# Optimization experiments

Hardware: AMD Instinct MI355X
Metric: run time of the kernel (lower is better)

The kernel has to match this reference:

```python
import jax, jax.numpy as jnp
import numpy as np

NEIGHBORS_FOR_LRF = 128
NEIGHBORS_FOR_AVG = 128
EPS = 1e-12  # safe-sqrt epsilon (self-distance is exactly 0)


def _pairwise_dist(v):
    # v: [N, 3] -> [N, N] euclidean distances
    sq = jnp.sum(v * v, axis=-1)
    d2 = sq[:, None] - 2.0 * (v @ v.T) + sq[None, :]
    return jnp.sqrt(jnp.maximum(d2, EPS))


def _shot_lrf(neighborhoods, radius):
    # neighborhoods: [N, K, 3] (centered at query point); radius: [N]
    d = jnp.sqrt(jnp.maximum(jnp.sum(neighborhoods * neighborhoods, axis=-1), EPS))  # [N, K]
    w = radius[:, None] - d  # SHOT weights (radius - distance)
    cov = jnp.einsum("nk,nki,nkj->nij", w, neighborhoods, neighborhoods)
    cov = cov / jnp.sum(w, axis=-1)[:, None, None]  # [N, 3, 3]
    _, vecs = jnp.linalg.eigh(cov)  # ascending eigenvalues; eigenvectors in columns
    x = vecs[:, :, 2]  # largest-eigenvalue direction
    z = vecs[:, :, 0]  # smallest-eigenvalue direction (normal)
    # SHOT sign disambiguation: orient toward the majority of neighbors
    xp = jnp.einsum("nki,ni->nk", neighborhoods, x)
    x = jnp.where((jnp.sum(xp >= 0, axis=-1) >= jnp.sum(xp < 0, axis=-1))[:, None], x, -x)
    zp = jnp.einsum("nki,ni->nk", neighborhoods, z)
    z = jnp.where((jnp.sum(zp >= 0, axis=-1) >= jnp.sum(zp < 0, axis=-1))[:, None], z, -z)
    y = jnp.cross(z, x)
    return jnp.stack([z, y, x], axis=1)  # [N, 3, 3]; row 0 = normal


def _per_sample(v):
    # v: [N, 3]
    D = _pairwise_dist(v)  # [N, N]
    neg_d, idx = jax.lax.top_k(-D, NEIGHBORS_FOR_LRF)  # nearest K (incl. self)
    radii = -neg_d  # [N, K], ascending distances
    radius = radii[:, -1]  # per-neighborhood support radius
    neighborhoods = v[idx] - v[:, None, :]  # [N, K, 3]
    lrfs = _shot_lrf(neighborhoods, radius)
    normals = lrfs[:, 0, :]  # [N, 3]
    avg = jnp.mean(normals[idx[:, :NEIGHBORS_FOR_AVG]], axis=1)  # gather + mean
    return avg / jnp.linalg.norm(avg, axis=-1, keepdims=True)


def setup_inputs() -> dict:
    key = jax.random.key(0)
    vertices = jax.random.normal(key, (2, 8192, 3), dtype=jnp.float32)
    return {"vertices": vertices}


def reference(vertices) -> jnp.ndarray:
    # tf.map_fn over batch -> vmap
    return jax.vmap(_per_sample)(vertices)  # [B, N, 3] averaged unit normals
```

## Files before the change

kernel.cpp:

```cpp
#include <hip/hip_runtime.h>

#define NPTS 8192
#define KNN  128
#define TPB  256
#define WPB  4
#define CANDCAP 384


__device__ __forceinline__ float f_signf(float a, float b){ return copysignf(a, b); }

__device__ float lapy2f(float x, float y){
#pragma clang fp contract(off)
  float xa = fabsf(x), ya = fabsf(y);
  float w = fmaxf(xa, ya), zz = fminf(xa, ya);
  if (zz == 0.0f) return w;
  float t = zz / w;
  return w * sqrtf(1.0f + t * t);
}

__device__ void slartg_(float f, float g, float &c, float &s, float &r){
#pragma clang fp contract(off)
  const float safmin = 1.17549435e-38f;
  const float safmax = 8.5070592e37f;
  if (g == 0.0f){ c = 1.0f; s = 0.0f; r = f; }
  else if (f == 0.0f){ c = 0.0f; s = f_signf(1.0f, g); r = fabsf(g); }
  else {
    float f1 = fabsf(f), g1 = fabsf(g);
    float rtmin = sqrtf(safmin);
    float rtmax = sqrtf(safmax * 0.5f);
    if (f1 > rtmin && f1 < rtmax && g1 > rtmin && g1 < rtmax){
      float d = sqrtf(f * f + g * g);
      float p = 1.0f / d;
      c = f1 * p;
      s = g * f_signf(p, f);
      r = f_signf(d, f);
    } else {
      float u = fminf(safmax, fmaxf(safmin, fmaxf(f1, g1)));
      float uu = 1.0f / u;
      float fs = f * uu, gs = g * uu;
      float d = sqrtf(fs * fs + gs * gs);
      float p = 1.0f / d;
      c = fabsf(fs) * p;
      s = gs * f_signf(p, f);
      r = f_signf(d, f) * u;
    }
  }
}

__device__ void slaev2_(float a, float b, float cc, float &rt1, float &rt2,
                        float &cs1, float &sn1){
#pragma clang fp contract(off)
  float sm = a + cc;
  float df = a - cc;
  float adf = fabsf(df);
  float tb = b + b;
  float ab = fabsf(tb);
  float acmx, acmn;
  if (fabsf(a) > fabsf(cc)){ acmx = a; acmn = cc; } else { acmx = cc; acmn = a; }
  float rt;
  if (adf > ab){ float t = ab / adf; rt = adf * sqrtf(1.0f + t * t); }
  else if (adf < ab){ float t = adf / ab; rt = ab * sqrtf(1.0f + t * t); }
  else { rt = ab * sqrtf(2.0f); }
  int sgn1;
  if (sm < 0.0f){ rt1 = 0.5f * (sm - rt); sgn1 = -1; rt2 = (acmx / rt1) * acmn - (b / rt1) * b; }
  else if (sm > 0.0f){ rt1 = 0.5f * (sm + rt); sgn1 = 1; rt2 = (acmx / rt1) * acmn - (b / rt1) * b; }
  else { rt1 = 0.5f * rt; rt2 = -0.5f * rt; sgn1 = 1; }
  float cs; int sgn2;
  if (df >= 0.0f){ cs = df + rt; sgn2 = 1; }
  else { cs = df - rt; sgn2 = -1; }
  float acs = fabsf(cs);
  if (acs > ab){
    float ct = -tb / cs;
    sn1 = 1.0f / sqrtf(1.0f + ct * ct);
    cs1 = ct * sn1;
  } else {
    if (ab == 0.0f){ cs1 = 1.0f; sn1 = 0.0f; }
    else {
      float tn = -cs / tb;
      cs1 = 1.0f / sqrtf(1.0f + tn * tn);
      sn1 = tn * cs1;
    }
  }
  if (sgn1 == sgn2){ float tn = cs1; cs1 = -sn1; sn1 = tn; }
}

__device__ void ssteqr3(float *d, float *e, float z[3][3]){
#pragma clang fp contract(off)
  const float eps  = 5.9604645e-8f;
  const float eps2 = 3.5527137e-15f;
  const float safmin = 1.17549435e-38f;
  const int n = 3;
  for (int i = 0; i < 3; i++)
    for (int j = 0; j < 3; j++) z[i][j] = (i == j) ? 1.0f : 0.0f;
  const int nmaxit = n * 30;
  int jtot = 0;
  int l1 = 1;
  int l = 0, lsv = 0, lend = 0, lendsv = 0, m = 0;
  float p, g, r, c, s, f, b;
  float csave[2], ssave[2];
  int safety = 0;

L10:
  if (++safety > 64) goto L190;
  if (l1 > n) goto L160;
  if (l1 > 1) e[l1 - 2] = 0.0f;
  if (l1 <= n - 1){
    for (m = l1; m <= n - 1; m++){
      float tst = fabsf(e[m - 1]);
      if (tst == 0.0f) goto L30;
      if (tst <= (sqrtf(fabsf(d[m - 1])) * sqrtf(fabsf(d[m]))) * eps){ e[m - 1] = 0.0f; goto L30; }
    }
  }
  m = n;
L30:
  l = l1; lsv = l; lend = m; lendsv = lend; l1 = m + 1;
  if (lend == l) goto L10;
  {
    float anorm = fabsf(d[l - 1]);
    for (int q = l; q <= lend - 1; q++){
      anorm = fmaxf(anorm, fabsf(d[q]));
      anorm = fmaxf(anorm, fabsf(e[q - 1]));
    }
    if (anorm == 0.0f) goto L10;
  }
  if (fabsf(d[lend - 1]) < fabsf(d[l - 1])){ lend = lsv; l = lendsv; }
  if (lend > l){
L40:
    if (l != lend){
      for (m = l; m <= lend - 1; m++){
        float tst = e[m - 1] * e[m - 1];
        if (tst <= (eps2 * fabsf(d[m - 1])) * fabsf(d[m]) + safmin) goto L60;
      }
    }
    m = lend;
L60:
    if (m < lend) e[m - 1] = 0.0f;
    p = d[l - 1];
    if (m == l) goto L80;
    if (m == l + 1){
      float rt1, rt2;
      slaev2_(d[l - 1], e[l - 1], d[l], rt1, rt2, c, s);
      for (int i2 = 0; i2 < 3; i2++){
        float temp = z[i2][l];
        z[i2][l]     = c * temp - s * z[i2][l - 1];
        z[i2][l - 1] = s * temp + c * z[i2][l - 1];
      }
      d[l - 1] = rt1; d[l] = rt2; e[l - 1] = 0.0f;
      l += 2;
      if (l <= lend) goto L40;
      goto L140;
    }
    if (jtot == nmaxit) goto L140;
    jtot++;
    g = (d[l] - p) / (2.0f * e[l - 1]);
    r = lapy2f(g, 1.0f);
    g = d[m - 1] - p + e[l - 1] / (g + f_signf(r, g));
    s = 1.0f; c = 1.0f; p = 0.0f;
    for (int i2 = m - 1; i2 >= l; i2--){
      f = s * e[i2 - 1];
      b = c * e[i2 - 1];
      slartg_(g, f, c, s, r);
      if (i2 != m - 1) e[i2] = r;
      g = d[i2] - p;
      r = (d[i2 - 1] - g) * s + 2.0f * c * b;
      p = s * r;
      d[i2] = g + p;
      g = c * r - b;
      csave[i2 - l] = c; ssave[i2 - l] = -s;
    }
    {
      int mmc = m - l + 1;
      for (int j2 = mmc - 1; j2 >= 1; j2--){
        float cj = csave[j2 - 1], sj = ssave[j2 - 1];
        if (cj != 1.0f || sj != 0.0f){
          for (int i2 = 0; i2 < 3; i2++){
            float temp = z[i2][(l - 1) + j2];
            z[i2][(l - 1) + j2]     = cj * temp - sj * z[i2][(l - 1) + j2 - 1];
            z[i2][(l - 1) + j2 - 1] = sj * temp + cj * z[i2][(l - 1) + j2 - 1];
          }
        }
      }
    }
    d[l - 1] -= p;
    e[l - 1] = g;
    goto L40;
L80:
    d[l - 1] = p;
    l++;
    if (l <= lend) goto L40;
    goto L140;
  } else {
L90:
    if (l != lend){
      for (m = l; m >= lend + 1; m--){
        float tst = e[m - 2] * e[m - 2];
        if (tst <= (eps2 * fabsf(d[m - 1])) * fabsf(d[m - 2]) + safmin) goto L110;
      }
    }
    m = lend;
L110:
    if (m > lend) e[m - 2] = 0.0f;
    p = d[l - 1];
    if (m == l) goto L130;
    if (m == l - 1){
      float rt1, rt2;
      slaev2_(d[l - 2], e[l - 2], d[l - 1], rt1, rt2, c, s);
      for (int i2 = 0; i2 < 3; i2++){
        float temp = z[i2][l - 1];
        z[i2][l - 1] = c * temp - s * z[i2][l - 2];
        z[i2][l - 2] = s * temp + c * z[i2][l - 2];
      }
      d[l - 2] = rt1; d[l - 1] = rt2; e[l - 2] = 0.0f;
      l -= 2;
      if (l >= lend) goto L90;
      goto L140;
    }
    if (jtot == nmaxit) goto L140;
    jtot++;
    g = (d[l - 2] - p) / (2.0f * e[l - 2]);
    r = lapy2f(g, 1.0f);
    g = d[m - 1] - p + e[l - 2] / (g + f_signf(r, g));
    s = 1.0f; c = 1.0f; p = 0.0f;
    for (int i2 = m; i2 <= l - 1; i2++){
      f = s * e[i2 - 1];
      b = c * e[i2 - 1];
      slartg_(g, f, c, s, r);
      if (i2 != m) e[i2 - 2] = r;
      g = d[i2 - 1] - p;
      r = (d[i2] - g) * s + 2.0f * c * b;
      p = s * r;
      d[i2 - 1] = g + p;
      g = c * r - b;
      csave[i2 - m] = c; ssave[i2 - m] = s;
    }
    {
      int cnt = l - m + 1;
      for (int j2 = 1; j2 <= cnt - 1; j2++){
        float cj = csave[j2 - 1], sj = ssave[j2 - 1];
        if (cj != 1.0f || sj != 0.0f){
          for (int i2 = 0; i2 < 3; i2++){
            float temp = z[i2][(m - 1) + j2];
            z[i2][(m - 1) + j2]     = cj * temp - sj * z[i2][(m - 1) + j2 - 1];
            z[i2][(m - 1) + j2 - 1] = sj * temp + cj * z[i2][(m - 1) + j2 - 1];
          }
        }
      }
    }
    d[l - 1] -= p;
    e[l - 2] = g;
    goto L90;
L130:
    d[l - 1] = p;
    l--;
    if (l >= lend) goto L90;
    goto L140;
  }
L140:
  if (jtot < nmaxit) goto L10;
  goto L190;
L160:
  for (int ii = 2; ii <= n; ii++){
    int i2 = ii - 1, k2 = i2;
    float pp = d[i2 - 1];
    for (int j2 = ii; j2 <= n; j2++){
      if (d[j2 - 1] < pp){ k2 = j2; pp = d[j2 - 1]; }
    }
    if (k2 != i2){
      d[k2 - 1] = d[i2 - 1]; d[i2 - 1] = pp;
      for (int r2 = 0; r2 < 3; r2++){
        float tt = z[r2][i2 - 1]; z[r2][i2 - 1] = z[r2][k2 - 1]; z[r2][k2 - 1] = tt;
      }
    }
  }
L190: ;
}

__device__ void eigh3_smallest_f32(const float A6[6], float zout[3]){
#pragma clang fp contract(off)
  float a00 = A6[0], a10 = A6[1], a20 = A6[2], a11 = A6[3], a21 = A6[4], a22 = A6[5];
  float d[3], e[2], tau1 = 0.0f, v2 = 0.0f;
  float xnorm = fabsf(a20);
  if (xnorm == 0.0f){
    tau1 = 0.0f;
    d[0] = a00; d[1] = a11; d[2] = a22; e[0] = a10; e[1] = a21;
  } else {
    float alpha = a10;
    float beta = -f_signf(lapy2f(alpha, xnorm), alpha);
    tau1 = (beta - alpha) / beta;
    float rsc = 1.0f / (alpha - beta);
    v2 = a20 * rsc;
    float y1 = tau1 * a11 + tau1 * (a21 * v2);
    float y2 = tau1 * a21 + (tau1 * v2) * a22;
    float dotv = y1 + y2 * v2;
    float al = (-0.5f * tau1) * dotv;
    float w1 = y1 + al;
    float w2 = y2 + al * v2;
    d[0] = a00;
    d[1] = (a11 + (-w1)) + (w1 * (-1.0f));
    e[1] = (a21 + v2 * (-w1)) + (w2 * (-1.0f));
    d[2] = (a22 + v2 * (-w2)) + (w2 * (-v2));
    e[0] = beta;
  }
  float z[3][3];
  ssteqr3(d, e, z);
  if (tau1 != 0.0f){
    for (int j = 0; j < 3; j++){
      float wj = z[1][j] + z[2][j] * v2;
      float tmp = (-tau1) * wj;
      z[1][j] = z[1][j] + tmp;
      z[2][j] = z[2][j] + v2 * tmp;
    }
  }
  zout[0] = z[0][0]; zout[1] = z[1][0]; zout[2] = z[2][0];
}

__device__ __forceinline__ void wsync(){
  asm volatile("s_waitcnt lgkmcnt(0)" ::: "memory");
}
__device__ __forceinline__ unsigned int wscan_incl(unsigned int v, int lane){
  #pragma unroll
  for (int off = 1; off < 64; off <<= 1){
    unsigned int n = (unsigned int)__shfl_up((int)v, off, 64);
    if (lane >= off) v += n;
  }
  return v;
}
__device__ __forceinline__ unsigned int lanepos(unsigned long long bal){
  return __builtin_amdgcn_mbcnt_hi((unsigned int)(bal >> 32),
         __builtin_amdgcn_mbcnt_lo((unsigned int)bal, 0u));
}

#define DBITS(A_, B_, C_, SQJ_, OUT_) { \
  float dot_ = fmaf(vz, (C_), fmaf(vy, (B_), vx * (A_))); \
  float d2_ = (sqi - 2.0f * dot_) + (SQJ_); \
  float D_ = sqrtf(fmaxf(d2_, 1e-12f)); \
  OUT_ = __float_as_uint(D_); }

__global__ __launch_bounds__(256) void sq_kernel(const float* __restrict__ verts,
                                                 float* __restrict__ sqbuf, int total)
{
#pragma clang fp contract(off)
  int g = blockIdx.x * 256 + threadIdx.x;
  if (g < total){
    float a = verts[3 * g + 0], b = verts[3 * g + 1], c = verts[3 * g + 2];
    sqbuf[g] = (a * a + b * b) + c * c;
  }
}

__global__ __launch_bounds__(TPB, 8) void phase1_kernel(const float* __restrict__ verts,
                                                        const float* __restrict__ sqbuf,
                                                        float* __restrict__ normals,
                                                        unsigned short* __restrict__ idx_out)
{
#pragma clang fp contract(off)
  __shared__ unsigned long long regionA[WPB][CANDCAP];
  __shared__ float4 regionB[WPB][KNN];

  const int t    = threadIdx.x;
  const int w    = t >> 6;
  const int lane = t & 63;
  const int gq   = blockIdx.x * WPB + w;
  const int smp  = gq >> 13;
  const int i    = gq & (NPTS - 1);
  const float* V  = verts + (size_t)smp * NPTS * 3;
  const float* SQ = sqbuf + (size_t)smp * NPTS;

  unsigned long long* cand = &regionA[w][0];
  unsigned int* hist = (unsigned int*)cand;
  unsigned long long* skey = (unsigned long long*)&regionB[w][0];
  float4* nbf = &regionB[w][0];

  const float vx = V[3 * i + 0], vy = V[3 * i + 1], vz = V[3 * i + 2];
  const float sqi = SQ[i];

  unsigned int prefix = 0u, kt = KNN, cnt = 0u;
  int shift = 19, pshift = 32, stop_shift = 19;
  for (int level = 0; level < 4; level++){
    #pragma unroll
    for (int z2 = 0; z2 < 8; z2++) hist[z2 * 64 + lane] = 0u;
    wsync();
    const unsigned int dmask = (unsigned int)((1 << (pshift - shift)) - 1);
    #pragma unroll 2
    for (int k = 0; k < NPTS / 256; k++){
      const int j0 = k * 256 + lane * 4;
      const float4* Vp = (const float4*)(V + 3 * j0);
      float4 fa = Vp[0], fb = Vp[1], fc = Vp[2];
      float4 sj = *(const float4*)(SQ + j0);
      float px[4] = {fa.x, fa.w, fb.z, fc.y};
      float py[4] = {fa.y, fb.x, fb.w, fc.z};
      float pz[4] = {fa.z, fb.y, fc.x, fc.w};
      float ps[4] = {sj.x, sj.y, sj.z, sj.w};
      #pragma unroll
      for (int s = 0; s < 4; s++){
        unsigned int bits; DBITS(px[s], py[s], pz[s], ps[s], bits);
        if (level == 0){
          int v = (int)(bits >> 19) - 1696;
          unsigned int dig = (unsigned int)(v < 0 ? 0 : (v > 511 ? 511 : v));
          atomicAdd(&hist[dig], 1u);
        } else if ((bits >> pshift) == prefix){
          atomicAdd(&hist[(bits >> shift) & dmask], 1u);
        }
      }
    }
    wsync();
    unsigned int hh[8], inc[8], tot[8];
    #pragma unroll
    for (int s = 0; s < 8; s++){
      hh[s] = hist[s * 64 + lane];
      inc[s] = wscan_incl(hh[s], lane);
      tot[s] = (unsigned int)__shfl((int)inc[s], 63, 64);
    }
    unsigned int selb = 0xffffffffu, nkt = 0u, ncnt = 0u, basep = 0u;
    #pragma unroll
    for (int s = 0; s < 8; s++){
      unsigned int gincl = inc[s] + basep;
      unsigned int gexcl = gincl - hh[s];
      if (hh[s] > 0u && gexcl < kt && kt <= gincl){
        selb = (unsigned int)(s * 64 + lane); nkt = kt - gexcl; ncnt = hh[s];
      }
      basep += tot[s];
    }
    unsigned long long bal = __ballot(selb != 0xffffffffu);
    int src = (int)(__ffsll((long long)bal) - 1);
    selb = (unsigned int)__shfl((int)selb, src, 64);
    nkt  = (unsigned int)__shfl((int)nkt,  src, 64);
    ncnt = (unsigned int)__shfl((int)ncnt, src, 64);
    prefix = (level == 0) ? (selb + 1696u) : ((prefix << (pshift - shift)) | selb);
    kt = nkt; cnt = ncnt; stop_shift = shift;
    if (cnt <= 256u) break;
    pshift = shift;
    shift = (shift == 19) ? 11 : ((shift == 11) ? 3 : 0);
  }

  unsigned int base = 0u;
  #pragma unroll 2
  for (int k = 0; k < NPTS / 256; k++){
    const int j0 = k * 256 + lane * 4;
    const float4* Vp = (const float4*)(V + 3 * j0);
    float4 fa = Vp[0], fb = Vp[1], fc = Vp[2];
    float4 sj = *(const float4*)(SQ + j0);
    float px[4] = {fa.x, fa.w, fb.z, fc.y};
    float py[4] = {fa.y, fb.x, fb.w, fc.z};
    float pz[4] = {fa.z, fb.y, fc.x, fc.w};
    float ps[4] = {sj.x, sj.y, sj.z, sj.w};
    #pragma unroll
    for (int s = 0; s < 4; s++){
      unsigned int bits; DBITS(px[s], py[s], pz[s], ps[s], bits);
      bool pred = ((bits >> stop_shift) <= prefix);
      unsigned long long bal = __ballot(pred);
      if (pred){
        unsigned int p = base + lanepos(bal);
        if (p < CANDCAP) cand[p] = (((unsigned long long)bits) << 13) | (unsigned long long)(j0 + s);
      }
      base += (unsigned int)__popcll(bal);
    }
  }
  wsync();
  unsigned int candN = base; if (candN > CANDCAP) candN = CANDCAP;

  for (unsigned int c = lane; c < candN; c += 64){
    unsigned long long key = cand[c];
    unsigned int rank = 0u;
    #pragma unroll 4
    for (unsigned int jj = 0; jj < candN; jj++) rank += (cand[jj] < key) ? 1u : 0u;
    if (rank < KNN) skey[rank] = key;
  }
  wsync();

  const float radius = __uint_as_float((unsigned int)(skey[KNN - 1] >> 13));
  unsigned long long k0 = skey[lane];
  unsigned long long k1 = skey[lane + 64];
  wsync();
  {
    int j0 = (int)(k0 & 8191ULL);
    float a = V[3 * j0 + 0] - vx;
    float b = V[3 * j0 + 1] - vy;
    float c = V[3 * j0 + 2] - vz;
    float dd2 = (a * a + b * b) + c * c;
    nbf[lane] = make_float4(a, b, c, radius - sqrtf(fmaxf(dd2, 1e-12f)));
    idx_out[(size_t)gq * KNN + lane] = (unsigned short)j0;
  }
  {
    int j1 = (int)(k1 & 8191ULL);
    float a = V[3 * j1 + 0] - vx;
    float b = V[3 * j1 + 1] - vy;
    float c = V[3 * j1 + 2] - vz;
    float dd2 = (a * a + b * b) + c * c;
    nbf[lane + 64] = make_float4(a, b, c, radius - sqrtf(fmaxf(dd2, 1e-12f)));
    idx_out[(size_t)gq * KNN + 64 + lane] = (unsigned short)j1;
  }
  wsync();

  float acc = 0.0f;
  if (lane < 6){
    #pragma unroll 4
    for (int k = 0; k < KNN; k++){
      float4 nb4 = nbf[k];
      float wn = nb4.w, x = nb4.x, y = nb4.y, zc = nb4.z;
      float u = (lane == 0) ? x : ((lane == 1 || lane == 3) ? y : zc);
      float v = (lane < 3) ? x : ((lane < 5) ? y : zc);
      acc += (wn * u) * v;
    }
  } else if (lane == 6){
    float r8[8];
    for (int q = 0; q < 8; q++) r8[q] = nbf[q].w;
    for (int k = 8; k < KNN; k += 8)
      for (int q = 0; q < 8; q++) r8[q] += nbf[k + q].w;
    acc = ((r8[0] + r8[1]) + (r8[2] + r8[3])) + ((r8[4] + r8[5]) + (r8[6] + r8[7]));
  }
  float c00 = __shfl(acc, 0, 64), c10 = __shfl(acc, 1, 64), c20 = __shfl(acc, 2, 64);
  float c11 = __shfl(acc, 3, 64), c21 = __shfl(acc, 4, 64), c22 = __shfl(acc, 5, 64);
  float wsum = __shfl(acc, 6, 64);

  float A6[6];
  A6[0] = c00 / wsum; A6[1] = c10 / wsum; A6[2] = c20 / wsum;
  A6[3] = c11 / wsum; A6[4] = c21 / wsum; A6[5] = c22 / wsum;
  float zv[3];
  eigh3_smallest_f32(A6, zv);

  float4 q0 = nbf[lane], q1 = nbf[lane + 64];
  float zp0 = ((q0.x * zv[0]) + (q0.y * zv[1])) + (q0.z * zv[2]);
  float zp1 = ((q1.x * zv[0]) + (q1.y * zv[1])) + (q1.z * zv[2]);
  unsigned int votes = (unsigned int)__popcll(__ballot(zp0 >= 0.0f))
                     + (unsigned int)__popcll(__ballot(zp1 >= 0.0f));
  float sg = (votes >= (unsigned)(KNN - votes)) ? 1.0f : -1.0f;
  if (lane == 0){
    normals[(size_t)gq * 3 + 0] = sg * zv[0];
    normals[(size_t)gq * 3 + 1] = sg * zv[1];
    normals[(size_t)gq * 3 + 2] = sg * zv[2];
  }
}

__global__ __launch_bounds__(TPB) void phase2_kernel(const float* __restrict__ normals,
                                                     const unsigned short* __restrict__ idx_in,
                                                     float* __restrict__ out)
{
#pragma clang fp contract(off)
  const int t    = threadIdx.x;
  const int w    = t >> 6;
  const int lane = t & 63;
  const int g    = blockIdx.x * WPB + w;
  const int smp  = g >> 13;
  const int base = smp << 13;
  const int j0 = (int)idx_in[(size_t)g * KNN + lane];
  const int j1 = (int)idx_in[(size_t)g * KNN + 64 + lane];
  const float* n0 = normals + (size_t)(base + j0) * 3;
  const float* n1 = normals + (size_t)(base + j1) * 3;
  float a0 = n0[0] + n1[0];
  float a1 = n0[1] + n1[1];
  float a2 = n0[2] + n1[2];
  #pragma unroll
  for (int off = 32; off > 0; off >>= 1){
    a0 += __shfl_down(a0, off, 64);
    a1 += __shfl_down(a1, off, 64);
    a2 += __shfl_down(a2, off, 64);
  }
  if (lane == 0){
    a0 /= 128.0f; a1 /= 128.0f; a2 /= 128.0f;
    float nrm = sqrtf(((a0 * a0) + (a1 * a1)) + (a2 * a2));
    out[(size_t)g * 3 + 0] = a0 / nrm;
    out[(size_t)g * 3 + 1] = a1 / nrm;
    out[(size_t)g * 3 + 2] = a2 / nrm;
  }
}

extern "C" void kernel_launch(void* const* d_in, const int* in_sizes, int n_in,
                              void* d_out, int out_size, void* d_ws, size_t ws_size,
                              hipStream_t stream){
  const float* verts = (const float*)d_in[0];
  float* out = (float*)d_out;
  const int total = in_sizes[0] / 3;
  float* normals = (float*)d_ws;
  unsigned short* idxb = (unsigned short*)((char*)d_ws + (size_t)total * 3 * sizeof(float));
  float* sqbuf = (float*)((char*)d_ws + (size_t)total * 3 * sizeof(float)
                                       + (size_t)total * KNN * sizeof(unsigned short));
  sq_kernel<<<dim3((total + 255) / 256), dim3(256), 0, stream>>>(verts, sqbuf, total);
  phase1_kernel<<<dim3(total / WPB), dim3(TPB), 0, stream>>>(verts, sqbuf, normals, idxb);
  phase2_kernel<<<dim3(total / WPB), dim3(TPB), 0, stream>>>(normals, idxb, out);
}
```

Before: 269.5 us.

## Stage candidate point tiles in shared memory across block warps

Each block now cooperatively loads 1024-point tiles of vertices and squared norms into shared memory, and all four warps scan them from LDS instead of each warp streaming the full point set from global memory. The radix-select histogram passes and the candidate-collection pass both use the tiles. This needs block-wide barriers per tile and a block-level vote so all warps keep looping until every warp has finished selection. The cost is extra syncs, warps that have finished still joining tile loads, and 16KB more shared memory, which may lower occupancy.

```diff
diff --git a/kernel.cpp b/kernel.cpp
--- a/kernel.cpp
+++ b/kernel.cpp
@@ -4,6 +4,7 @@
 #define KNN  128
 #define TPB  256
 #define WPB  4
+#define TILE 1024
 #define CANDCAP 384
 
 
@@ -353,8 +354,10 @@
                                                         unsigned short* __restrict__ idx_out)
 {
 #pragma clang fp contract(off)
+  __shared__ float4 tileMem[TILE];
   __shared__ unsigned long long regionA[WPB][CANDCAP];
   __shared__ float4 regionB[WPB][KNN];
+  __shared__ unsigned int sh_cont;
 
   const int t    = threadIdx.x;
   const int w    = t >> 6;
@@ -364,6 +367,8 @@
   const int i    = gq & (NPTS - 1);
   const float* V  = verts + (size_t)smp * NPTS * 3;
   const float* SQ = sqbuf + (size_t)smp * NPTS;
+  const float* tV  = (const float*)tileMem;
+  const float* tSQ = (const float*)tileMem + 3 * TILE;
 
   unsigned long long* cand = &regionA[w][0];
   unsigned int* hist = (unsigned int*)cand;
@@ -375,17 +380,108 @@
 
   unsigned int prefix = 0u, kt = KNN, cnt = 0u;
   int shift = 19, pshift = 32, stop_shift = 19;
+  bool done = false;
   for (int level = 0; level < 4; level++){
+    if (!done){
+      #pragma unroll
+      for (int z2 = 0; z2 < 8; z2++) hist[z2 * 64 + lane] = 0u;
+    }
+    const unsigned int dmask = (unsigned int)((1 << (pshift - shift)) - 1);
+    for (int tb = 0; tb < NPTS; tb += TILE){
+      __syncthreads();
+      {
+        const float4* vsrc = (const float4*)(V + 3 * tb);
+        const float4* qsrc = (const float4*)(SQ + tb);
+        tileMem[t]       = vsrc[t];
+        tileMem[256 + t] = vsrc[256 + t];
+        tileMem[512 + t] = vsrc[512 + t];
+        tileMem[768 + t] = qsrc[t];
+      }
+      __syncthreads();
+      if (!done){
+        #pragma unroll
+        for (int k = 0; k < TILE / 256; k++){
+          const int j0 = k * 256 + lane * 4;
+          const float4* Vp = (const float4*)(tV + 3 * j0);
+          float4 fa = Vp[0], fb = Vp[1], fc = Vp[2];
+          float4 sj = *(const float4*)(tSQ + j0);
+          float px[4] = {fa.x, fa.w, fb.z, fc.y};
+          float py[4] = {fa.y, fb.x, fb.w, fc.z};
+          float pz[4] = {fa.z, fb.y, fc.x, fc.w};
+          float ps[4] = {sj.x, sj.y, sj.z, sj.w};
+          #pragma unroll
+          for (int s = 0; s < 4; s++){
+            unsigned int bits; DBITS(px[s], py[s], pz[s], ps[s], bits);
+            if (level == 0){
+              int v = (int)(bits >> 19) - 1696;
+              unsigned int dig = (unsigned int)(v < 0 ? 0 : (v > 511 ? 511 : v));
+              atomicAdd(&hist[dig], 1u);
+            } else if ((bits >> pshift) == prefix){
+              atomicAdd(&hist[(bits >> shift) & dmask], 1u);
+            }
+          }
+        }
+      }
+    }
+    if (!done){
+      wsync();
+      unsigned int hh[8], inc[8], tot[8];
+      #pragma unroll
+      for (int s = 0; s < 8; s++){
+        hh[s] = hist[s * 64 + lane];
+        inc[s] = wscan_incl(hh[s], lane);
+        tot[s] = (unsigned int)__shfl((int)inc[s], 63, 64);
+      }
+      unsigned int selb = 0xffffffffu, nkt = 0u, ncnt = 0u, basep = 0u;
+      #pragma unroll
+      for (int s = 0; s < 8; s++){
+        unsigned int gincl = inc[s] + basep;
+        unsigned int gexcl = gincl - hh[s];
+        if (hh[s] > 0u && gexcl < kt && kt <= gincl){
+          selb = (unsigned int)(s * 64 + lane); nkt = kt - gexcl; ncnt = hh[s];
+        }
+        basep += tot[s];
+      }
+      unsigned long long bal = __ballot(selb != 0xffffffffu);
+      int src = (int)(__ffsll((long long)bal) - 1);
+      selb = (unsigned int)__shfl((int)selb, src, 64);
+      nkt  = (unsigned int)__shfl((int)nkt,  src, 64);
+      ncnt = (unsigned int)__shfl((int)ncnt, src, 64);
+      prefix = (level == 0) ? (selb + 1696u) : ((prefix << (pshift - shift)) | selb);
+      kt = nkt; cnt = ncnt; stop_shift = shift;
+      if (cnt <= 256u || level == 3){
+        done = true;
+      } else {
+        pshift = shift;
+        shift = (shift == 19) ? 11 : ((shift == 11) ? 3 : 0);
+      }
+    }
+    if (t == 0) sh_cont = 0u;
+    __syncthreads();
+    if (!done && lane == 0) atomicAdd(&sh_cont, 1u);
+    __syncthreads();
+    if (sh_cont == 0u) break;
+  }
+  (void)cnt;
+
+  unsigned int base = 0u;
+  for (int tb = 0; tb < NPTS; tb += TILE){
+    __syncthreads();
+    {
+      const float4* vsrc = (const float4*)(V + 3 * tb);
+      const float4* qsrc = (const float4*)(SQ + tb);
+      tileMem[t]       = vsrc[t];
+      tileMem[256 + t] = vsrc[256 + t];
+      tileMem[512 + t] = vsrc[512 + t];
+      tileMem[768 + t] = qsrc[t];
+    }
+    __syncthreads();
     #pragma unroll
-    for (int z2 = 0; z2 < 8; z2++) hist[z2 * 64 + lane] = 0u;
-    wsync();
-    const unsigned int dmask = (unsigned int)((1 << (pshift - shift)) - 1);
-    #pragma unroll 2
-    for (int k = 0; k < NPTS / 256; k++){
+    for (int k = 0; k < TILE / 256; k++){
       const int j0 = k * 256 + lane * 4;
-      const float4* Vp = (const float4*)(V + 3 * j0);
+      const float4* Vp = (const float4*)(tV + 3 * j0);
       float4 fa = Vp[0], fb = Vp[1], fc = Vp[2];
-      float4 sj = *(const float4*)(SQ + j0);
+      float4 sj = *(const float4*)(tSQ + j0);
       float px[4] = {fa.x, fa.w, fb.z, fc.y};
       float py[4] = {fa.y, fb.x, fb.w, fc.z};
       float pz[4] = {fa.z, fb.y, fc.x, fc.w};
@@ -393,66 +489,14 @@
       #pragma unroll
       for (int s = 0; s < 4; s++){
         unsigned int bits; DBITS(px[s], py[s], pz[s], ps[s], bits);
-        if (level == 0){
-          int v = (int)(bits >> 19) - 1696;
-          unsigned int dig = (unsigned int)(v < 0 ? 0 : (v > 511 ? 511 : v));
-          atomicAdd(&hist[dig], 1u);
-        } else if ((bits >> pshift) == prefix){
-          atomicAdd(&hist[(bits >> shift) & dmask], 1u);
+        bool pred = ((bits >> stop_shift) <= prefix);
+        unsigned long long bal = __ballot(pred);
+        if (pred){
+          unsigned int p = base + lanepos(bal);
+          if (p < CANDCAP) cand[p] = (((unsigned long long)bits) << 13) | (unsigned long long)(tb + j0 + s);
         }
-      }
-    }
-    wsync();
-    unsigned int hh[8], inc[8], tot[8];
-    #pragma unroll
-    for (int s = 0; s < 8; s++){
-      hh[s] = hist[s * 64 + lane];
-      inc[s] = wscan_incl(hh[s], lane);
-      tot[s] = (unsigned int)__shfl((int)inc[s], 63, 64);
-    }
-    unsigned int selb = 0xffffffffu, nkt = 0u, ncnt = 0u, basep = 0u;
-    #pragma unroll
-    for (int s = 0; s < 8; s++){
-      unsigned int gincl = inc[s] + basep;
-      unsigned int gexcl = gincl - hh[s];
-      if (hh[s] > 0u && gexcl < kt && kt <= gincl){
-        selb = (unsigned int)(s * 64 + lane); nkt = kt - gexcl; ncnt = hh[s];
-      }
-      basep += tot[s];
-    }
-    unsigned long long bal = __ballot(selb != 0xffffffffu);
-    int src = (int)(__ffsll((long long)bal) - 1);
-    selb = (unsigned int)__shfl((int)selb, src, 64);
-    nkt  = (unsigned int)__shfl((int)nkt,  src, 64);
-    ncnt = (unsigned int)__shfl((int)ncnt, src, 64);
-    prefix = (level == 0) ? (selb + 1696u) : ((prefix << (pshift - shift)) | selb);
-    kt = nkt; cnt = ncnt; stop_shift = shift;
-    if (cnt <= 256u) break;
-    pshift = shift;
-    shift = (shift == 19) ? 11 : ((shift == 11) ? 3 : 0);
-  }
-
-  unsigned int base = 0u;
-  #pragma unroll 2
-  for (int k = 0; k < NPTS / 256; k++){
-    const int j0 = k * 256 + lane * 4;
-    const float4* Vp = (const float4*)(V + 3 * j0);
-    float4 fa = Vp[0], fb = Vp[1], fc = Vp[2];
-    float4 sj = *(const float4*)(SQ + j0);
-    float px[4] = {fa.x, fa.w, fb.z, fc.y};
-    float py[4] = {fa.y, fb.x, fb.w, fc.z};
-    float pz[4] = {fa.z, fb.y, fc.x, fc.w};
-    float ps[4] = {sj.x, sj.y, sj.z, sj.w};
-    #pragma unroll
-    for (int s = 0; s < 4; s++){
-      unsigned int bits; DBITS(px[s], py[s], pz[s], ps[s], bits);
-      bool pred = ((bits >> stop_shift) <= prefix);
-      unsigned long long bal = __ballot(pred);
-      if (pred){
-        unsigned int p = base + lanepos(bal);
-        if (p < CANDCAP) cand[p] = (((unsigned long long)bits) << 13) | (unsigned long long)(j0 + s);
-      }
-      base += (unsigned int)__popcll(bal);
+        base += (unsigned int)__popcll(bal);
+      }
     }
   }
   wsync();
```

Result: slower. 336.2 us (+24.7%).

## Process two query points per wavefront to share candidate vertex loads

Applied to the files above, without the earlier changes.

Each wavefront now computes distances for two query points at once, reusing every loaded vertex and squared-norm value for both queries during the radix-select histogram passes and the candidate collection pass. Histograms are placed in the second shared region so both queries have separate buffers, and the post-selection work runs sequentially per query. This aims to halve global/L2 load traffic per query and raise instruction-level parallelism, at the cost of doubled shared memory per block, lower launch-bound occupancy, and level loops that run until both queries finish.

```diff
diff --git a/kernel.cpp b/kernel.cpp
--- a/kernel.cpp
+++ b/kernel.cpp
@@ -4,6 +4,8 @@
 #define KNN  128
 #define TPB  256
 #define WPB  4
+#define QPW  2
+#define QPB  (WPB*QPW)
 #define CANDCAP 384
 
 
@@ -330,9 +332,9 @@
          __builtin_amdgcn_mbcnt_lo((unsigned int)bal, 0u));
 }
 
-#define DBITS(A_, B_, C_, SQJ_, OUT_) { \
-  float dot_ = fmaf(vz, (C_), fmaf(vy, (B_), vx * (A_))); \
-  float d2_ = (sqi - 2.0f * dot_) + (SQJ_); \
+#define DBITS(VX_, VY_, VZ_, SQI_, A_, B_, C_, SQJ_, OUT_) { \
+  float dot_ = fmaf((VZ_), (C_), fmaf((VY_), (B_), (VX_) * (A_))); \
+  float d2_ = ((SQI_) - 2.0f * dot_) + (SQJ_); \
   float D_ = sqrtf(fmaxf(d2_, 1e-12f)); \
   OUT_ = __float_as_uint(D_); }
 
@@ -347,37 +349,48 @@
   }
 }
 
-__global__ __launch_bounds__(TPB, 8) void phase1_kernel(const float* __restrict__ verts,
+__global__ __launch_bounds__(TPB, 4) void phase1_kernel(const float* __restrict__ verts,
                                                         const float* __restrict__ sqbuf,
                                                         float* __restrict__ normals,
                                                         unsigned short* __restrict__ idx_out)
 {
 #pragma clang fp contract(off)
-  __shared__ unsigned long long regionA[WPB][CANDCAP];
-  __shared__ float4 regionB[WPB][KNN];
+  __shared__ unsigned long long regionA[QPB][CANDCAP];
+  __shared__ float4 regionB[QPB][KNN];
 
   const int t    = threadIdx.x;
   const int w    = t >> 6;
   const int lane = t & 63;
-  const int gq   = blockIdx.x * WPB + w;
-  const int smp  = gq >> 13;
-  const int i    = gq & (NPTS - 1);
+  const int gq0  = blockIdx.x * QPB + w * QPW;
+  const int smp  = gq0 >> 13;
+  const int i0   = gq0 & (NPTS - 1);
+  const int i1   = i0 + 1;
   const float* V  = verts + (size_t)smp * NPTS * 3;
   const float* SQ = sqbuf + (size_t)smp * NPTS;
 
-  unsigned long long* cand = &regionA[w][0];
-  unsigned int* hist = (unsigned int*)cand;
-  unsigned long long* skey = (unsigned long long*)&regionB[w][0];
-  float4* nbf = &regionB[w][0];
-
-  const float vx = V[3 * i + 0], vy = V[3 * i + 1], vz = V[3 * i + 2];
-  const float sqi = SQ[i];
-
-  unsigned int prefix = 0u, kt = KNN, cnt = 0u;
-  int shift = 19, pshift = 32, stop_shift = 19;
+  const int q0 = w * QPW, q1 = q0 + 1;
+  unsigned long long* candQ[2] = { &regionA[q0][0], &regionA[q1][0] };
+  unsigned int* histQ[2] = { (unsigned int*)&regionB[q0][0], (unsigned int*)&regionB[q1][0] };
+
+  const float vx0 = V[3 * i0 + 0], vy0 = V[3 * i0 + 1], vz0 = V[3 * i0 + 2];
+  const float vx1 = V[3 * i1 + 0], vy1 = V[3 * i1 + 1], vz1 = V[3 * i1 + 2];
+  const float sqi0 = SQ[i0], sqi1 = SQ[i1];
+
+  unsigned int pre[2] = {0u, 0u};
+  unsigned int kt[2] = {KNN, KNN};
+  int stop[2] = {19, 19};
+  bool done[2] = {false, false};
+  const int SH[4] = {19, 11, 3, 0};
+  const int PS[4] = {32, 19, 11, 3};
   for (int level = 0; level < 4; level++){
+    const int shift = SH[level], pshift = PS[level];
     #pragma unroll
-    for (int z2 = 0; z2 < 8; z2++) hist[z2 * 64 + lane] = 0u;
+    for (int q = 0; q < 2; q++){
+      if (!done[q]){
+        #pragma unroll
+        for (int z2 = 0; z2 < 8; z2++) histQ[q][z2 * 64 + lane] = 0u;
+      }
+    }
     wsync();
     const unsigned int dmask = (unsigned int)((1 << (pshift - shift)) - 1);
     #pragma unroll 2
@@ -392,47 +405,58 @@
       float ps[4] = {sj.x, sj.y, sj.z, sj.w};
       #pragma unroll
       for (int s = 0; s < 4; s++){
-        unsigned int bits; DBITS(px[s], py[s], pz[s], ps[s], bits);
+        unsigned int bits0, bits1;
+        DBITS(vx0, vy0, vz0, sqi0, px[s], py[s], pz[s], ps[s], bits0);
+        DBITS(vx1, vy1, vz1, sqi1, px[s], py[s], pz[s], ps[s], bits1);
         if (level == 0){
-          int v = (int)(bits >> 19) - 1696;
-          unsigned int dig = (unsigned int)(v < 0 ? 0 : (v > 511 ? 511 : v));
-          atomicAdd(&hist[dig], 1u);
-        } else if ((bits >> pshift) == prefix){
-          atomicAdd(&hist[(bits >> shift) & dmask], 1u);
+          int v0 = (int)(bits0 >> 19) - 1696;
+          int v1 = (int)(bits1 >> 19) - 1696;
+          atomicAdd(&histQ[0][(unsigned int)(v0 < 0 ? 0 : (v0 > 511 ? 511 : v0))], 1u);
+          atomicAdd(&histQ[1][(unsigned int)(v1 < 0 ? 0 : (v1 > 511 ? 511 : v1))], 1u);
+        } else {
+          if (!done[0] && (bits0 >> pshift) == pre[0])
+            atomicAdd(&histQ[0][(bits0 >> shift) & dmask], 1u);
+          if (!done[1] && (bits1 >> pshift) == pre[1])
+            atomicAdd(&histQ[1][(bits1 >> shift) & dmask], 1u);
         }
       }
     }
     wsync();
-    unsigned int hh[8], inc[8], tot[8];
     #pragma unroll
-    for (int s = 0; s < 8; s++){
-      hh[s] = hist[s * 64 + lane];
-      inc[s] = wscan_incl(hh[s], lane);
-      tot[s] = (unsigned int)__shfl((int)inc[s], 63, 64);
-    }
-    unsigned int selb = 0xffffffffu, nkt = 0u, ncnt = 0u, basep = 0u;
-    #pragma unroll
-    for (int s = 0; s < 8; s++){
-      unsigned int gincl = inc[s] + basep;
-      unsigned int gexcl = gincl - hh[s];
-      if (hh[s] > 0u && gexcl < kt && kt <= gincl){
-        selb = (unsigned int)(s * 64 + lane); nkt = kt - gexcl; ncnt = hh[s];
-      }
-      basep += tot[s];
-    }
-    unsigned long long bal = __ballot(selb != 0xffffffffu);
-    int src = (int)(__ffsll((long long)bal) - 1);
-    selb = (unsigned int)__shfl((int)selb, src, 64);
-    nkt  = (unsigned int)__shfl((int)nkt,  src, 64);
-    ncnt = (unsigned int)__shfl((int)ncnt, src, 64);
-    prefix = (level == 0) ? (selb + 1696u) : ((prefix << (pshift - shift)) | selb);
-    kt = nkt; cnt = ncnt; stop_shift = shift;
-    if (cnt <= 256u) break;
-    pshift = shift;
-    shift = (shift == 19) ? 11 : ((shift == 11) ? 3 : 0);
-  }
-
-  unsigned int base = 0u;
+    for (int q = 0; q < 2; q++){
+      if (done[q]) continue;
+      unsigned int hh[8], inc[8], tot[8];
+      #pragma unroll
+      for (int s = 0; s < 8; s++){
+        hh[s] = histQ[q][s * 64 + lane];
+        inc[s] = wscan_incl(hh[s], lane);
+        tot[s] = (unsigned int)__shfl((int)inc[s], 63, 64);
+      }
+      unsigned int selb = 0xffffffffu, nkt = 0u, ncnt = 0u, basep = 0u;
+      #pragma unroll
+      for (int s = 0; s < 8; s++){
+        unsigned int gincl = inc[s] + basep;
+        unsigned int gexcl = gincl - hh[s];
+        if (hh[s] > 0u && gexcl < kt[q] && kt[q] <= gincl){
+          selb = (unsigned int)(s * 64 + lane); nkt = kt[q] - gexcl; ncnt = hh[s];
+        }
+        basep += tot[s];
+      }
+      unsigned long long bal = __ballot(selb != 0xffffffffu);
+      int src = (int)(__ffsll((long long)bal) - 1);
+      selb = (unsigned int)__shfl((int)selb, src, 64);
+      nkt  = (unsigned int)__shfl((int)nkt,  src, 64);
+      ncnt = (unsigned int)__shfl((int)ncnt, src, 64);
+      pre[q] = (level == 0) ? (selb + 1696u) : ((pre[q] << (pshift - shift)) | selb);
+      kt[q] = nkt; stop[q] = shift;
+      if (ncnt <= 256u || level == 3) done[q] = true;
+    }
+    if (done[0] && done[1]) break;
+  }
+
+  unsigned int base0 = 0u, base1 = 0u;
+  const int st0 = stop[0], st1 = stop[1];
+  const unsigned int P0 = pre[0], P1 = pre[1];
   #pragma unroll 2
   for (int k = 0; k < NPTS / 256; k++){
     const int j0 = k * 256 + lane * 4;
@@ -445,89 +469,111 @@
     float ps[4] = {sj.x, sj.y, sj.z, sj.w};
     #pragma unroll
     for (int s = 0; s < 4; s++){
-      unsigned int bits; DBITS(px[s], py[s], pz[s], ps[s], bits);
-      bool pred = ((bits >> stop_shift) <= prefix);
-      unsigned long long bal = __ballot(pred);
-      if (pred){
-        unsigned int p = base + lanepos(bal);
-        if (p < CANDCAP) cand[p] = (((unsigned long long)bits) << 13) | (unsigned long long)(j0 + s);
-      }
-      base += (unsigned int)__popcll(bal);
+      unsigned int bits0, bits1;
+      DBITS(vx0, vy0, vz0, sqi0, px[s], py[s], pz[s], ps[s], bits0);
+      DBITS(vx1, vy1, vz1, sqi1, px[s], py[s], pz[s], ps[s], bits1);
+      bool pr0 = ((bits0 >> st0) <= P0);
+      bool pr1 = ((bits1 >> st1) <= P1);
+      unsigned long long bal0 = __ballot(pr0);
+      unsigned long long bal1 = __ballot(pr1);
+      if (pr0){
+        unsigned int p = base0 + lanepos(bal0);
+        if (p < CANDCAP) candQ[0][p] = (((unsigned long long)bits0) << 13) | (unsigned long long)(j0 + s);
+      }
+      if (pr1){
+        unsigned int p = base1 + lanepos(bal1);
+        if (p < CANDCAP) candQ[1][p] = (((unsigned long long)bits1) << 13) | (unsigned long long)(j0 + s);
+      }
+      base0 += (unsigned int)__popcll(bal0);
+      base1 += (unsigned int)__popcll(bal1);
     }
   }
   wsync();
-  unsigned int candN = base; if (candN > CANDCAP) candN = CANDCAP;
-
-  for (unsigned int c = lane; c < candN; c += 64){
-    unsigned long long key = cand[c];
-    unsigned int rank = 0u;
-    #pragma unroll 4
-    for (unsigned int jj = 0; jj < candN; jj++) rank += (cand[jj] < key) ? 1u : 0u;
-    if (rank < KNN) skey[rank] = key;
-  }
-  wsync();
-
-  const float radius = __uint_as_float((unsigned int)(skey[KNN - 1] >> 13));
-  unsigned long long k0 = skey[lane];
-  unsigned long long k1 = skey[lane + 64];
-  wsync();
-  {
-    int j0 = (int)(k0 & 8191ULL);
-    float a = V[3 * j0 + 0] - vx;
-    float b = V[3 * j0 + 1] - vy;
-    float c = V[3 * j0 + 2] - vz;
-    float dd2 = (a * a + b * b) + c * c;
-    nbf[lane] = make_float4(a, b, c, radius - sqrtf(fmaxf(dd2, 1e-12f)));
-    idx_out[(size_t)gq * KNN + lane] = (unsigned short)j0;
-  }
-  {
-    int j1 = (int)(k1 & 8191ULL);
-    float a = V[3 * j1 + 0] - vx;
-    float b = V[3 * j1 + 1] - vy;
-    float c = V[3 * j1 + 2] - vz;
-    float dd2 = (a * a + b * b) + c * c;
-    nbf[lane + 64] = make_float4(a, b, c, radius - sqrtf(fmaxf(dd2, 1e-12f)));
-    idx_out[(size_t)gq * KNN + 64 + lane] = (unsigned short)j1;
-  }
-  wsync();
-
-  float acc = 0.0f;
-  if (lane < 6){
-    #pragma unroll 4
-    for (int k = 0; k < KNN; k++){
-      float4 nb4 = nbf[k];
-      float wn = nb4.w, x = nb4.x, y = nb4.y, zc = nb4.z;
-      float u = (lane == 0) ? x : ((lane == 1 || lane == 3) ? y : zc);
-      float v = (lane < 3) ? x : ((lane < 5) ? y : zc);
-      acc += (wn * u) * v;
-    }
-  } else if (lane == 6){
-    float r8[8];
-    for (int q = 0; q < 8; q++) r8[q] = nbf[q].w;
-    for (int k = 8; k < KNN; k += 8)
-      for (int q = 0; q < 8; q++) r8[q] += nbf[k + q].w;
-    acc = ((r8[0] + r8[1]) + (r8[2] + r8[3])) + ((r8[4] + r8[5]) + (r8[6] + r8[7]));
-  }
-  float c00 = __shfl(acc, 0, 64), c10 = __shfl(acc, 1, 64), c20 = __shfl(acc, 2, 64);
-  float c11 = __shfl(acc, 3, 64), c21 = __shfl(acc, 4, 64), c22 = __shfl(acc, 5, 64);
-  float wsum = __shfl(acc, 6, 64);
-
-  float A6[6];
-  A6[0] = c00 / wsum; A6[1] = c10 / wsum; A6[2] = c20 / wsum;
-  A6[3] = c11 / wsum; A6[4] = c21 / wsum; A6[5] = c22 / wsum;
-  float zv[3];
-  eigh3_smallest_f32(A6, zv);
-
-  float4 q0 = nbf[lane], q1 = nbf[lane + 64];
-  float zp0 = ((q0.x * zv[0]) + (q0.y * zv[1])) + (q0.z * zv[2]);
-  float zp1 = ((q1.x * zv[0]) + (q1.y * zv[1])) + (q1.z * zv[2]);
-  unsigned int votes = (unsigned int)__popcll(__ballot(zp0 >= 0.0f))
-                     + (unsigned int)__popcll(__ballot(zp1 >= 0.0f));
-  float sg = (votes >= (unsigned)(KNN - votes)) ? 1.0f : -1.0f;
-  if (lane == 0){
-    normals[(size_t)gq * 3 + 0] = sg * zv[0];
-    normals[(size_t)gq * 3 + 1] = sg * zv[1];
-    normals[(size_t)gq * 3 + 2] = sg * zv[2];
+
+  #pragma unroll
+  for (int q = 0; q < 2; q++){
+    const int gq = gq0 + q;
+    unsigned long long* cand = candQ[q];
+    unsigned long long* skey = (unsigned long long*)&regionB[w * QPW + q][0];
+    float4* nbf = &regionB[w * QPW + q][0];
+    const float vx = (q == 0) ? vx0 : vx1;
+    const float vy = (q == 0) ? vy0 : vy1;
+    const float vz = (q == 0) ? vz0 : vz1;
+    unsigned int candN = (q == 0) ? base0 : base1;
+    if (candN > CANDCAP) candN = CANDCAP;
+
+    for (unsigned int c = lane; c < candN; c += 64){
+      unsigned long long key = cand[c];
+      unsigned int rank = 0u;
+      #pragma unroll 4
+      for (unsigned int jj = 0; jj < candN; jj++) rank += (cand[jj] < key) ? 1u : 0u;
+      if (rank < KNN) skey[rank] = key;
+    }
+    wsync();
+
+    const float radius = __uint_as_float((unsigned int)(skey[KNN - 1] >> 13));
+    unsigned long long k0 = skey[lane];
+    unsigned long long k1 = skey[lane + 64];
+    wsync();
+    {
+      int j0 = (int)(k0 & 8191ULL);
+      float a = V[3 * j0 + 0] - vx;
+      float b = V[3 * j0 + 1] - vy;
+      float c = V[3 * j0 + 2] - vz;
+      float dd2 = (a * a + b * b) + c * c;
+      nbf[lane] = make_float4(a, b, c, radius - sqrtf(fmaxf(dd2, 1e-12f)));
+      idx_out[(size_t)gq * KNN + lane] = (unsigned short)j0;
+    }
+    {
+      int j1 = (int)(k1 & 8191ULL);
+      float a = V[3 * j1 + 0] - vx;
+      float b = V[3 * j1 + 1] - vy;
+      float c = V[3 * j1 + 2] - vz;
+      float dd2 = (a * a + b * b) + c * c;
+      nbf[lane + 64] = make_float4(a, b, c, radius - sqrtf(fmaxf(dd2, 1e-12f)));
+      idx_out[(size_t)gq * KNN + 64 + lane] = (unsigned short)j1;
+    }
+    wsync();
+
+    float acc = 0.0f;
+    if (lane < 6){
+      #pragma unroll 4
+      for (int k = 0; k < KNN; k++){
+        float4 nb4 = nbf[k];
+        float wn = nb4.w, x = nb4.x, y = nb4.y, zc = nb4.z;
+        float u = (lane == 0) ? x : ((lane == 1 || lane == 3) ? y : zc);
+        float v = (lane < 3) ? x : ((lane < 5) ? y : zc);
+        acc += (wn * u) * v;
+      }
+    } else if (lane == 6){
+      float r8[8];
+      for (int qq = 0; qq < 8; qq++) r8[qq] = nbf[qq].w;
+      for (int k = 8; k < KNN; k += 8)
+        for (int qq = 0; qq < 8; qq++) r8[qq] += nbf[k + qq].w;
+      acc = ((r8[0] + r8[1]) + (r8[2] + r8[3])) + ((r8[4] + r8[5]) + (r8[6] + r8[7]));
+    }
+    float c00 = __shfl(acc, 0, 64), c10 = __shfl(acc, 1, 64), c20 = __shfl(acc, 2, 64);
+    float c11 = __shfl(acc, 3, 64), c21 = __shfl(acc, 4, 64), c22 = __shfl(acc, 5, 64);
+    float wsum = __shfl(acc, 6, 64);
+
+    float A6[6];
+    A6[0] = c00 / wsum; A6[1] = c10 / wsum; A6[2] = c20 / wsum;
+    A6[3] = c11 / wsum; A6[4] = c21 / wsum; A6[5] = c22 / wsum;
+    float zv[3];
+    eigh3_smallest_f32(A6, zv);
+
+    float4 f0 = nbf[lane], f1 = nbf[lane + 64];
+    float zp0 = ((f0.x * zv[0]) + (f0.y * zv[1])) + (f0.z * zv[2]);
+    float zp1 = ((f1.x * zv[0]) + (f1.y * zv[1])) + (f1.z * zv[2]);
+    unsigned int votes = (unsigned int)__popcll(__ballot(zp0 >= 0.0f))
+                       + (unsigned int)__popcll(__ballot(zp1 >= 0.0f));
+    float sg = (votes >= (unsigned)(KNN - votes)) ? 1.0f : -1.0f;
+    if (lane == 0){
+      normals[(size_t)gq * 3 + 0] = sg * zv[0];
+      normals[(size_t)gq * 3 + 1] = sg * zv[1];
+      normals[(size_t)gq * 3 + 2] = sg * zv[2];
+    }
+    wsync();
   }
 }
 
@@ -575,6 +621,6 @@
   float* sqbuf = (float*)((char*)d_ws + (size_t)total * 3 * sizeof(float)
                                        + (size_t)total * KNN * sizeof(unsigned short));
   sq_kernel<<<dim3((total + 255) / 256), dim3(256), 0, stream>>>(verts, sqbuf, total);
-  phase1_kernel<<<dim3(total / WPB), dim3(TPB), 0, stream>>>(verts, sqbuf, normals, idxb);
+  phase1_kernel<<<dim3(total / QPB), dim3(TPB), 0, stream>>>(verts, sqbuf, normals, idxb);
   phase2_kernel<<<dim3(total / WPB), dim3(TPB), 0, stream>>>(normals, idxb, out);
 }
```

New measurement: 312.7 us. +16.0%, slower.
